# Optimization experiments

Hardware: AMD Instinct MI355X
Metric: run time of the kernel (lower is better)

The kernel has to match this reference:

```python
import jax, jax.numpy as jnp
import numpy as np

EMB = 512   # embedding_dim
HID = 512   # hidden_dim
UNITS = 512 # attention units
BS = 1024
SEQ = 360


def setup_inputs() -> dict:
    key = jax.random.key(0)
    k1, k2, k3, k4, k5, k6, k7, k8 = jax.random.split(key, 8)
    s_w1 = 1.0 / np.sqrt(EMB)
    s_w2 = 1.0 / np.sqrt(HID)
    s_v = 1.0 / np.sqrt(UNITS)
    return {
        "hidden": jax.random.normal(k1, (1, BS, HID), dtype=jnp.float32),
        "features": jax.random.normal(k2, (BS, SEQ, EMB), dtype=jnp.float32),
        "W1_w": jax.random.uniform(k3, (UNITS, EMB), jnp.float32, -s_w1, s_w1),
        "W1_b": jax.random.uniform(k4, (UNITS,), jnp.float32, -s_w1, s_w1),
        "W2_w": jax.random.uniform(k5, (UNITS, HID), jnp.float32, -s_w2, s_w2),
        "W2_b": jax.random.uniform(k6, (UNITS,), jnp.float32, -s_w2, s_w2),
        "V_w": jax.random.uniform(k7, (1, UNITS), jnp.float32, -s_v, s_v),
        "V_b": jax.random.uniform(k8, (1,), jnp.float32, -s_v, s_v),
    }


def reference(hidden, features, W1_w, W1_b, W2_w, W2_b, V_w, V_b):
    # hidden: [1, bs, hid] -> [bs, 1, hid]
    hidden_t = jnp.swapaxes(hidden, 0, 1)
    # W1(features): [bs, seq, units]; W2(hidden): [bs, 1, units]
    f_proj = jax.nn.relu(jnp.einsum('bse,ue->bsu', features, W1_w) + W1_b)
    h_proj = jax.nn.relu(jnp.einsum('boh,uh->bou', hidden_t, W2_w) + W2_b)
    attn_hidden = jnp.tanh(f_proj + h_proj)              # [bs, seq, units]
    score = jnp.einsum('bsu,ou->bso', attn_hidden, V_w) + V_b  # [bs, seq, 1]
    attention_weights = jax.nn.softmax(score, axis=1)    # softmax over seq
    context_vector = jnp.sum(attention_weights * features, axis=1)  # [bs, emb]
    return (context_vector, attention_weights)
```

## Files before the change

kernel.cpp:

```cpp
#include <hip/hip_runtime.h>
#include <hip/hip_bf16.h>

#define EMB 512
#define HID 512
#define UNITS 512
#define BS 1024
#define SEQ 360

typedef __attribute__((ext_vector_type(4))) float f32x4;
typedef __attribute__((ext_vector_type(8))) short bf16x8;

__device__ __forceinline__ unsigned int pk2bf(float lo, float hi) {
    unsigned int ulo = __float_as_uint(lo);
    unsigned int uhi = __float_as_uint(hi);
    ulo += 0x7fffu + ((ulo >> 16) & 1u);
    uhi += 0x7fffu + ((uhi >> 16) & 1u);
    return (ulo >> 16) | (uhi & 0xffff0000u);
}

__global__ __launch_bounds__(256) void k_convert_w1(const float* __restrict__ w1,
                                                    unsigned short* __restrict__ w1bf) {
    int i = (blockIdx.x * 256 + threadIdx.x) * 4;
    float4 v = *(const float4*)(w1 + i);
    uint2 o;
    o.x = pk2bf(v.x, v.y);
    o.y = pk2bf(v.z, v.w);
    *(uint2*)(w1bf + i) = o;
}

__global__ __launch_bounds__(256) void k_hproj(const float* __restrict__ hidden,
                                               const float* __restrict__ w2,
                                               const float* __restrict__ b2,
                                               float* __restrict__ hp) {
    __shared__ float hid[4 * 512];
    int t = threadIdx.x;
    int b0 = blockIdx.x * 4;
    const float4* src = (const float4*)(hidden + (size_t)b0 * 512);
    ((float4*)hid)[t * 2] = src[t * 2];
    ((float4*)hid)[t * 2 + 1] = src[t * 2 + 1];
    __syncthreads();
    int u0 = t, u1 = t + 256;
    float acc0[4] = {0.f, 0.f, 0.f, 0.f};
    float acc1[4] = {0.f, 0.f, 0.f, 0.f};
    const float4* w2_0 = (const float4*)(w2 + (size_t)u0 * 512);
    const float4* w2_1 = (const float4*)(w2 + (size_t)u1 * 512);
    const float4* h4 = (const float4*)hid;
    for (int k = 0; k < 128; ++k) {
        float4 a = w2_0[k];
        float4 c = w2_1[k];
#pragma unroll
        for (int bb = 0; bb < 4; ++bb) {
            float4 hv = h4[bb * 128 + k];
            acc0[bb] += a.x * hv.x + a.y * hv.y + a.z * hv.z + a.w * hv.w;
            acc1[bb] += c.x * hv.x + c.y * hv.y + c.z * hv.z + c.w * hv.w;
        }
    }
    float bias0 = b2[u0], bias1 = b2[u1];
#pragma unroll
    for (int bb = 0; bb < 4; ++bb) {
        hp[(size_t)(b0 + bb) * 512 + u0] = fmaxf(acc0[bb] + bias0, 0.f);
        hp[(size_t)(b0 + bb) * 512 + u1] = fmaxf(acc1[bb] + bias1, 0.f);
    }
}

#define MT 64
#define KT 64

__global__ __launch_bounds__(256, 2) void k_score(const float* __restrict__ F,
                                                  const unsigned short* __restrict__ W1bf,
                                                  const float* __restrict__ b1,
                                                  const float* __restrict__ hp,
                                                  const float* __restrict__ Vw,
                                                  float* __restrict__ scores) {
    __shared__ uint4 lsA[MT * 8];
    __shared__ float lds_part[4][MT];

    int t = threadIdx.x;
    int wave = t >> 6, lane = t & 63;
    int col = lane & 15, quad = lane >> 4;
    int tile = blockIdx.x % 6;
    int b = blockIdx.x / 6;
    int s0 = tile * MT;

    f32x4 acc[4][8];
#pragma unroll
    for (int mb = 0; mb < 4; ++mb)
#pragma unroll
        for (int nb = 0; nb < 8; ++nb) {
            f32x4 z = {0.f, 0.f, 0.f, 0.f};
            acc[mb][nb] = z;
        }

    int srow = t >> 2;
    int kpi = t & 3;
    int sIdx = s0 + srow;
    if (sIdx > 359) sIdx = 359;
    const float* Fr = F + ((size_t)(b * 360 + sIdx) * 512 + kpi * 16);
    int sw = srow & 7;
    int c0 = (2 * kpi) ^ sw;
    int c1 = (2 * kpi + 1) ^ sw;
    uint4* wdst0 = &lsA[srow * 8 + c0];
    uint4* wdst1 = &lsA[srow * 8 + c1];

    int uBase = wave * 128 + col;
    int cw = col & 7;

    float4 a0 = *(const float4*)(Fr);
    float4 a1 = *(const float4*)(Fr + 4);
    float4 a2 = *(const float4*)(Fr + 8);
    float4 a3 = *(const float4*)(Fr + 12);

#pragma unroll
    for (int k0 = 0; k0 < 512; k0 += KT) {
        uint4 u0, u1;
        u0.x = pk2bf(a0.x, a0.y); u0.y = pk2bf(a0.z, a0.w);
        u0.z = pk2bf(a1.x, a1.y); u0.w = pk2bf(a1.z, a1.w);
        u1.x = pk2bf(a2.x, a2.y); u1.y = pk2bf(a2.z, a2.w);
        u1.z = pk2bf(a3.x, a3.y); u1.w = pk2bf(a3.z, a3.w);
        __syncthreads();
        *wdst0 = u0;
        *wdst1 = u1;
        float4 n0 = {0.f,0.f,0.f,0.f}, n1 = n0, n2 = n0, n3 = n0;
        if (k0 + KT < 512) {
            const float* Fn = Fr + k0 + KT;
            n0 = *(const float4*)(Fn);
            n1 = *(const float4*)(Fn + 4);
            n2 = *(const float4*)(Fn + 8);
            n3 = *(const float4*)(Fn + 12);
        }
        __syncthreads();
#pragma unroll
        for (int kk = 0; kk < KT; kk += 32) {
            int kkc = kk >> 3;
            bf16x8 bfrag[8];
#pragma unroll
            for (int nb = 0; nb < 8; ++nb)
                bfrag[nb] = *(const bf16x8*)&W1bf[(size_t)(uBase + nb * 16) * 512 + k0 + kk + quad * 8];
            bf16x8 afrag[4];
#pragma unroll
            for (int mb = 0; mb < 4; ++mb)
                afrag[mb] = *(const bf16x8*)&lsA[(mb * 16 + col) * 8 + ((kkc + quad) ^ cw)];
#pragma unroll
            for (int nb = 0; nb < 8; ++nb)
#pragma unroll
                for (int mb = 0; mb < 4; ++mb)
                    acc[mb][nb] = __builtin_amdgcn_mfma_f32_16x16x32_bf16(afrag[mb], bfrag[nb], acc[mb][nb], 0, 0, 0);
        }
        a0 = n0; a1 = n1; a2 = n2; a3 = n3;
    }

    float b1v[8], hpv[8], vv[8];
    float sumv = 0.f;
#pragma unroll
    for (int nb = 0; nb < 8; ++nb) {
        int u = uBase + nb * 16;
        b1v[nb] = b1[u];
        hpv[nb] = hp[(size_t)b * 512 + u];
        vv[nb] = Vw[u];
        sumv += vv[nb];
    }
#pragma unroll
    for (int mb = 0; mb < 4; ++mb) {
#pragma unroll
        for (int r = 0; r < 4; ++r) {
            float p2 = 0.f;
#pragma unroll
            for (int nb = 0; nb < 8; ++nb) {
                float x = fmaxf(acc[mb][nb][r] + b1v[nb], 0.f) + hpv[nb];
                float e = __builtin_amdgcn_exp2f(x * 2.885390082f);
                float rc = __builtin_amdgcn_rcpf(e + 1.0f);
                p2 += vv[nb] * rc;
            }
            float p = sumv - 2.0f * p2;
            p += __shfl_xor(p, 1);
            p += __shfl_xor(p, 2);
            p += __shfl_xor(p, 4);
            p += __shfl_xor(p, 8);
            if (col == 0) lds_part[wave][mb * 16 + quad * 4 + r] = p;
        }
    }
    __syncthreads();
    if (t < MT) {
        float s = lds_part[0][t] + lds_part[1][t] + lds_part[2][t] + lds_part[3][t];
        int sg = s0 + t;
        if (sg < 360) scores[(size_t)b * 360 + sg] = s;
    }
}

__global__ __launch_bounds__(256) void k_softctx(const float* __restrict__ F,
                                                 const float* __restrict__ scores,
                                                 float* __restrict__ outc,
                                                 float* __restrict__ outw) {
    __shared__ float wL[SEQ];
    __shared__ float red[8];
    __shared__ f32x4 red8[8][32];
    int t = threadIdx.x;
    int b = blockIdx.x >> 2;
    int chunk = blockIdx.x & 3;
    int lane = t & 63, wid = t >> 6;

    float sa = (t < SEQ) ? scores[(size_t)b * SEQ + t] : -1e30f;
    float sb = (t + 256 < SEQ) ? scores[(size_t)b * SEQ + t + 256] : -1e30f;
    float m = fmaxf(sa, sb);
#pragma unroll
    for (int off = 32; off; off >>= 1) m = fmaxf(m, __shfl_xor(m, off));
    if (lane == 0) red[wid] = m;
    __syncthreads();
    m = fmaxf(fmaxf(red[0], red[1]), fmaxf(red[2], red[3]));

    const float L2E = 1.4426950408889634f;
    float e0 = (t < SEQ) ? __builtin_amdgcn_exp2f((sa - m) * L2E) : 0.f;
    float e1 = (t + 256 < SEQ) ? __builtin_amdgcn_exp2f((sb - m) * L2E) : 0.f;
    float sum = e0 + e1;
#pragma unroll
    for (int off = 32; off; off >>= 1) sum += __shfl_xor(sum, off);
    if (lane == 0) red[4 + wid] = sum;
    __syncthreads();
    float inv = 1.0f / (red[4] + red[5] + red[6] + red[7]);

    if (t < SEQ) {
        float w = e0 * inv;
        wL[t] = w;
        if (chunk == 0) outw[(size_t)b * SEQ + t] = w;
    }
    if (t + 256 < SEQ) {
        float w = e1 * inv;
        wL[t + 256] = w;
        if (chunk == 0) outw[(size_t)b * SEQ + t + 256] = w;
    }
    __syncthreads();

    int c4 = t & 31, strip = t >> 5;
    const f32x4* Fb = (const f32x4*)F + (size_t)b * SEQ * 128 + chunk * 32 + c4;
    f32x4 a = {0.f, 0.f, 0.f, 0.f};
    for (int s = strip; s < SEQ; s += 8) a += wL[s] * Fb[(size_t)s * 128];
    red8[strip][c4] = a;
    __syncthreads();
    if (t < 32) {
        f32x4 s = red8[0][t];
#pragma unroll
        for (int k = 1; k < 8; ++k) s += red8[k][t];
        ((f32x4*)outc)[(size_t)b * 128 + chunk * 32 + t] = s;
    }
}

extern "C" void kernel_launch(void* const* d_in, const int* in_sizes, int n_in,
                              void* d_out, int out_size, void* d_ws, size_t ws_size,
                              hipStream_t stream) {
    const float* hidden   = (const float*)d_in[0];
    const float* features = (const float*)d_in[1];
    const float* W1_w     = (const float*)d_in[2];
    const float* W1_b     = (const float*)d_in[3];
    const float* W2_w     = (const float*)d_in[4];
    const float* W2_b     = (const float*)d_in[5];
    const float* V_w      = (const float*)d_in[6];

    float* outc = (float*)d_out;
    float* outw = (float*)d_out + (size_t)BS * EMB;

    char* ws = (char*)d_ws;
    unsigned short* w1bf = (unsigned short*)ws;
    float* hp      = (float*)(ws + 524288);
    float* scoresW = (float*)(ws + 524288 + 2097152);

    hipLaunchKernelGGL(k_convert_w1, dim3(256), dim3(256), 0, stream, W1_w, w1bf);
    hipLaunchKernelGGL(k_hproj, dim3(256), dim3(256), 0, stream, hidden, W2_w, W2_b, hp);
    hipLaunchKernelGGL(k_score, dim3(BS * 6), dim3(256), 0, stream,
                       features, w1bf, W1_b, hp, V_w, scoresW);
    hipLaunchKernelGGL(k_softctx, dim3(BS * 4), dim3(256), 0, stream,
                       features, scoresW, outc, outw);
}
```

Before: 1.455 ms.

## Split score GEMM across unit halves and pre-swizzle W1 into fragment layout

Each k_score block now covers only half of the 512 attention units, which halves the accumulator registers and allows three blocks per CU instead of two. The grid doubles, and the two partial score sums are written to separate buffers that k_softctx adds together. W1 is converted to bf16 in an MFMA-fragment-ordered layout so each lane's B-fragment loads are contiguous 16-byte reads. The cost is that every features tile is now loaded and converted to bf16 twice, once per unit half, which doubles global feature reads in the score kernel.

```diff
diff --git a/kernel.cpp b/kernel.cpp
--- a/kernel.cpp
+++ b/kernel.cpp
@@ -19,13 +19,21 @@
 }
 
 __global__ __launch_bounds__(256) void k_convert_w1(const float* __restrict__ w1,
-                                                    unsigned short* __restrict__ w1bf) {
-    int i = (blockIdx.x * 256 + threadIdx.x) * 4;
-    float4 v = *(const float4*)(w1 + i);
-    uint2 o;
-    o.x = pk2bf(v.x, v.y);
-    o.y = pk2bf(v.z, v.w);
-    *(uint2*)(w1bf + i) = o;
+                                                    unsigned short* __restrict__ w1p) {
+    int t = blockIdx.x * 256 + threadIdx.x;
+    int u = t >> 6;
+    int eg = t & 63;
+    int e = eg << 3;
+    const float4* src = (const float4*)(w1 + (size_t)u * 512 + e);
+    float4 v0 = src[0], v1 = src[1];
+    uint4 o;
+    o.x = pk2bf(v0.x, v0.y);
+    o.y = pk2bf(v0.z, v0.w);
+    o.z = pk2bf(v1.x, v1.y);
+    o.w = pk2bf(v1.z, v1.w);
+    int g = u >> 4, col = u & 15;
+    int c = e >> 5, quad = (e >> 3) & 3;
+    ((uint4*)w1p)[((size_t)(g * 16 + c) * 64) + col * 4 + quad] = o;
 }
 
 __global__ __launch_bounds__(256) void k_hproj(const float* __restrict__ hidden,
@@ -66,27 +74,29 @@
 #define MT 64
 #define KT 64
 
-__global__ __launch_bounds__(256, 2) void k_score(const float* __restrict__ F,
-                                                  const unsigned short* __restrict__ W1bf,
+__global__ __launch_bounds__(256, 3) void k_score(const float* __restrict__ F,
+                                                  const unsigned short* __restrict__ W1p,
                                                   const float* __restrict__ b1,
                                                   const float* __restrict__ hp,
                                                   const float* __restrict__ Vw,
-                                                  float* __restrict__ scores) {
+                                                  float* __restrict__ scoresP) {
     __shared__ uint4 lsA[MT * 8];
     __shared__ float lds_part[4][MT];
 
     int t = threadIdx.x;
     int wave = t >> 6, lane = t & 63;
     int col = lane & 15, quad = lane >> 4;
-    int tile = blockIdx.x % 6;
-    int b = blockIdx.x / 6;
+    int half = blockIdx.x & 1;
+    int tb = blockIdx.x >> 1;
+    int tile = tb % 6;
+    int b = tb / 6;
     int s0 = tile * MT;
 
-    f32x4 acc[4][8];
+    f32x4 acc[4][4];
 #pragma unroll
     for (int mb = 0; mb < 4; ++mb)
 #pragma unroll
-        for (int nb = 0; nb < 8; ++nb) {
+        for (int nb = 0; nb < 4; ++nb) {
             f32x4 z = {0.f, 0.f, 0.f, 0.f};
             acc[mb][nb] = z;
         }
@@ -102,7 +112,8 @@
     uint4* wdst0 = &lsA[srow * 8 + c0];
     uint4* wdst1 = &lsA[srow * 8 + c1];
 
-    int uBase = wave * 128 + col;
+    int ugrp0 = half * 16 + wave * 4;
+    const unsigned short* Bbase = W1p + (size_t)ugrp0 * 8192 + (size_t)(col * 4 + quad) * 8;
     int cw = col & 7;
 
     float4 a0 = *(const float4*)(Fr);
@@ -132,16 +143,17 @@
 #pragma unroll
         for (int kk = 0; kk < KT; kk += 32) {
             int kkc = kk >> 3;
-            bf16x8 bfrag[8];
-#pragma unroll
-            for (int nb = 0; nb < 8; ++nb)
-                bfrag[nb] = *(const bf16x8*)&W1bf[(size_t)(uBase + nb * 16) * 512 + k0 + kk + quad * 8];
+            const unsigned short* Bk = Bbase + (size_t)(k0 + kk) * 16;
+            bf16x8 bfrag[4];
+#pragma unroll
+            for (int nb = 0; nb < 4; ++nb)
+                bfrag[nb] = *(const bf16x8*)(Bk + (size_t)nb * 8192);
             bf16x8 afrag[4];
 #pragma unroll
             for (int mb = 0; mb < 4; ++mb)
                 afrag[mb] = *(const bf16x8*)&lsA[(mb * 16 + col) * 8 + ((kkc + quad) ^ cw)];
 #pragma unroll
-            for (int nb = 0; nb < 8; ++nb)
+            for (int nb = 0; nb < 4; ++nb)
 #pragma unroll
                 for (int mb = 0; mb < 4; ++mb)
                     acc[mb][nb] = __builtin_amdgcn_mfma_f32_16x16x32_bf16(afrag[mb], bfrag[nb], acc[mb][nb], 0, 0, 0);
@@ -149,11 +161,12 @@
         a0 = n0; a1 = n1; a2 = n2; a3 = n3;
     }
 
-    float b1v[8], hpv[8], vv[8];
+    float b1v[4], hpv[4], vv[4];
     float sumv = 0.f;
-#pragma unroll
-    for (int nb = 0; nb < 8; ++nb) {
-        int u = uBase + nb * 16;
+    int uB = half * 256 + wave * 64 + col;
+#pragma unroll
+    for (int nb = 0; nb < 4; ++nb) {
+        int u = uB + nb * 16;
         b1v[nb] = b1[u];
         hpv[nb] = hp[(size_t)b * 512 + u];
         vv[nb] = Vw[u];
@@ -165,7 +178,7 @@
         for (int r = 0; r < 4; ++r) {
             float p2 = 0.f;
 #pragma unroll
-            for (int nb = 0; nb < 8; ++nb) {
+            for (int nb = 0; nb < 4; ++nb) {
                 float x = fmaxf(acc[mb][nb][r] + b1v[nb], 0.f) + hpv[nb];
                 float e = __builtin_amdgcn_exp2f(x * 2.885390082f);
                 float rc = __builtin_amdgcn_rcpf(e + 1.0f);
@@ -183,12 +196,13 @@
     if (t < MT) {
         float s = lds_part[0][t] + lds_part[1][t] + lds_part[2][t] + lds_part[3][t];
         int sg = s0 + t;
-        if (sg < 360) scores[(size_t)b * 360 + sg] = s;
+        if (sg < 360)
+            scoresP[(size_t)half * BS * SEQ + (size_t)b * SEQ + sg] = s;
     }
 }
 
 __global__ __launch_bounds__(256) void k_softctx(const float* __restrict__ F,
-                                                 const float* __restrict__ scores,
+                                                 const float* __restrict__ scoresP,
                                                  float* __restrict__ outc,
                                                  float* __restrict__ outw) {
     __shared__ float wL[SEQ];
@@ -199,8 +213,10 @@
     int chunk = blockIdx.x & 3;
     int lane = t & 63, wid = t >> 6;
 
-    float sa = (t < SEQ) ? scores[(size_t)b * SEQ + t] : -1e30f;
-    float sb = (t + 256 < SEQ) ? scores[(size_t)b * SEQ + t + 256] : -1e30f;
+    const float* sp0 = scoresP + (size_t)b * SEQ;
+    const float* sp1 = scoresP + (size_t)BS * SEQ + (size_t)b * SEQ;
+    float sa = (t < SEQ) ? (sp0[t] + sp1[t]) : -1e30f;
+    float sb = (t + 256 < SEQ) ? (sp0[t + 256] + sp1[t + 256]) : -1e30f;
     float m = fmaxf(sa, sb);
 #pragma unroll
     for (int off = 32; off; off >>= 1) m = fmaxf(m, __shfl_xor(m, off));
@@ -259,14 +275,14 @@
     float* outw = (float*)d_out + (size_t)BS * EMB;
 
     char* ws = (char*)d_ws;
-    unsigned short* w1bf = (unsigned short*)ws;
+    unsigned short* w1p = (unsigned short*)ws;
     float* hp      = (float*)(ws + 524288);
-    float* scoresW = (float*)(ws + 524288 + 2097152);
-
-    hipLaunchKernelGGL(k_convert_w1, dim3(256), dim3(256), 0, stream, W1_w, w1bf);
+    float* scoresP = (float*)(ws + 524288 + 2097152);
+
+    hipLaunchKernelGGL(k_convert_w1, dim3(128), dim3(256), 0, stream, W1_w, w1p);
     hipLaunchKernelGGL(k_hproj, dim3(256), dim3(256), 0, stream, hidden, W2_w, W2_b, hp);
-    hipLaunchKernelGGL(k_score, dim3(BS * 6), dim3(256), 0, stream,
-                       features, w1bf, W1_b, hp, V_w, scoresW);
+    hipLaunchKernelGGL(k_score, dim3(BS * 12), dim3(256), 0, stream,
+                       features, w1p, W1_b, hp, V_w, scoresP);
     hipLaunchKernelGGL(k_softctx, dim3(BS * 4), dim3(256), 0, stream,
-                       features, scoresW, outc, outw);
-}
+                       features, scoresP, outc, outw);
+}
```

Result: faster. 1.356 ms (-6.8%).
